# Kernel optimization log

Hardware: AMD Instinct MI355X
Metric: run time of the kernel (lower is better)

## Reference

```python
import jax, jax.numpy as jnp
import numpy as np

B, N, FH, H, FO = 8, 1024, 128, 8, 64
FIN = 2 * FH  # f_hid * 2
NEG = -1e9
SLOPE = 0.2  # leaky_relu negative slope (GAT default)


def setup_inputs() -> dict:
    key = jax.random.key(0)
    ks = jax.random.split(key, 10)
    x = jax.random.normal(ks[0], (B, FIN), jnp.float32)
    A = jax.random.randint(ks[1], (B, N, N), 0, 2, jnp.int32)  # 0/1 dense adjacency
    mask_zero = jnp.ones((B, N, 1), jnp.float32)  # node validity mask
    p_atten = jax.random.uniform(ks[2], (B, N), jnp.float32)  # unused in forward body
    e_atten = jax.random.uniform(ks[3], (B, N, FIN), jnp.float32)
    Npost = jax.random.normal(ks[4], (N, FIN), jnp.float32) * np.float32(1.0 / np.sqrt(FIN))  # kaiming-ish
    w = jax.random.normal(ks[5], (H, FIN, FO), jnp.float32) * np.float32(1.0 / np.sqrt(FIN))
    a_src = jax.random.normal(ks[6], (H, FO), jnp.float32) * np.float32(0.1)
    a_dst = jax.random.normal(ks[7], (H, FO), jnp.float32) * np.float32(0.1)
    bias = jnp.zeros((FO,), jnp.float32)
    return {"x": x, "A": A, "mask_zero": mask_zero, "p_atten": p_atten,
            "e_atten": e_atten, "Npost": Npost, "w": w, "a_src": a_src,
            "a_dst": a_dst, "bias": bias}


def reference(x, A, mask_zero, p_atten, e_atten, Npost, w, a_src, a_dst, bias):
    # broadcast-mul feature gating: x [B,FIN] repeated over N posts, gated by Npost*e_atten
    recx = x[:, None, :] * (Npost[None, :, :] * e_atten)          # [B,N,FIN]
    # BatchGAT (DeepInf-style multi-head graph attention, dropout disabled / eval mode)
    h = jnp.einsum('bnf,hfo->bhno', recx, w)                      # [B,H,N,FO]
    s = jnp.einsum('bhno,ho->bhn', h, a_src)                      # src attention term
    d = jnp.einsum('bhno,ho->bhn', h, a_dst)                      # dst attention term
    logits = jax.nn.leaky_relu(s[:, :, :, None] + d[:, :, None, :], SLOPE)  # [B,H,N,N]
    adj = (A > 0)[:, None, :, :]                                  # [B,1,N,N]
    logits = jnp.where(adj, logits, NEG)
    attn = jax.nn.softmax(logits, axis=-1)                        # masked row softmax
    out = jnp.einsum('bhnm,bhmo->bhno', attn, h) + bias           # aggregate neighbors
    out = out.mean(axis=1)                                        # average heads -> [B,N,FO]
    return out * mask_zero                                        # zero padded nodes
```

## Files before the change

kernel.cpp:

```cpp
#include <hip/hip_runtime.h>

typedef __attribute__((ext_vector_type(8))) short          bf16x8;
typedef __attribute__((ext_vector_type(8))) unsigned short u16x8;
typedef __attribute__((ext_vector_type(4))) unsigned short u16x4;
typedef __attribute__((ext_vector_type(4))) float          f32x4;
typedef __attribute__((ext_vector_type(4))) unsigned int   u32x4;

union U8 { u16x8 u; bf16x8 b; u32x4 w; };
union U4 { u16x4 u; unsigned w[2]; };

__device__ __forceinline__ unsigned short f2bf(float f){
  unsigned u = __float_as_uint(f);
  return (unsigned short)((u + 0x7fffu + ((u >> 16) & 1u)) >> 16);
}
__device__ __forceinline__ unsigned pack_bf16(float lo, float hi){
  unsigned a = __float_as_uint(hi) + 0x8000u;
  unsigned b = __float_as_uint(lo) + 0x8000u;
  return __builtin_amdgcn_perm(a, b, 0x07060302u);
}

#define NN  1024
#define FIN 256
#define NH  8
#define FO  64

__global__ __launch_bounds__(256) void stage0(
    const float* __restrict__ w, const int* __restrict__ A,
    const float* __restrict__ bias, const float* __restrict__ mz,
    unsigned short* __restrict__ wfrag, unsigned long long* __restrict__ Abits,
    float* __restrict__ out)
{
  const int tid = blockIdx.x * 256 + threadIdx.x;
  if (tid < 16384){
    const int lane = tid & 63, ss = (tid >> 6) & 3, kc = (tid >> 8) & 7, h = tid >> 11;
    const int o = 16 * ss + (lane & 15);
    const int f = kc * 32 + (lane >> 4) * 8;
    u16x8 r;
    #pragma unroll
    for (int j = 0; j < 8; j++) r[j] = f2bf(w[(h * FIN + f + j) * FO + o]);
    *(u16x8*)(wfrag + tid * 8) = r;
  }
  #pragma unroll
  for (int k = 0; k < 2; k++){
    const int i = tid + k * 262144;
    out[i] = bias[i & 63] * mz[i >> 6];
  }
  for (int i = tid; i < 8388608; i += 262144){
    unsigned long long m = __ballot(A[i] > 0);
    if ((threadIdx.x & 63) == 0) Abits[i >> 6] = m;
  }
}

__global__ __launch_bounds__(512, 4) void stageA(
    const float* __restrict__ x, const float* __restrict__ e_at,
    const float* __restrict__ Np, const unsigned short* __restrict__ wfrag,
    const float* __restrict__ a_src, const float* __restrict__ a_dst,
    unsigned short* __restrict__ hT,
    float* __restrict__ exps, float* __restrict__ exps2,
    float* __restrict__ expd, float* __restrict__ expd2)
{
  __shared__ unsigned short rex[16 * 264];
  const int t = threadIdx.x;
  const int n0 = blockIdx.x * 16, b = blockIdx.y;

  {
    const int row = t >> 5, f0 = (t & 31) * 8;
    const int nrow = n0 + row;
    const float* ep = e_at + (b * NN + nrow) * FIN + f0;
    const float* qp = Np + nrow * FIN + f0;
    const float* xp = x + b * FIN + f0;
    f32x4 e0 = *(const f32x4*)ep, e1 = *(const f32x4*)(ep + 4);
    f32x4 q0 = *(const f32x4*)qp, q1 = *(const f32x4*)(qp + 4);
    f32x4 x0 = *(const f32x4*)xp, x1 = *(const f32x4*)(xp + 4);
    u16x8 r;
    #pragma unroll
    for (int j = 0; j < 4; j++){
      r[j]     = f2bf(e0[j] * q0[j] * x0[j]);
      r[j + 4] = f2bf(e1[j] * q1[j] * x1[j]);
    }
    *(u16x8*)(rex + row * 264 + f0) = r;
  }
  __syncthreads();

  const int h = t >> 6, lane = t & 63, quad = lane >> 4, l15 = lane & 15;
  const unsigned short* wf = wfrag + h * 16384 + lane * 8;

  f32x4 acc[4] = {};
  #pragma unroll
  for (int kc = 0; kc < 8; kc++){
    U8 a0, bf[4];
    a0.u = *(const u16x8*)(rex + l15 * 264 + kc * 32 + quad * 8);
    #pragma unroll
    for (int ss = 0; ss < 4; ss++) bf[ss].u = *(const u16x8*)(wf + (kc * 4 + ss) * 512);
    #pragma unroll
    for (int ss = 0; ss < 4; ss++)
      acc[ss] = __builtin_amdgcn_mfma_f32_16x16x32_bf16(a0.b, bf[ss].b, acc[ss], 0, 0, 0);
  }

  {
    const int mtile = blockIdx.x >> 1, moff = (blockIdx.x & 1) * 16;
    unsigned short* pan = hT + (size_t)(((b * NH + h) * 32 + mtile) * 64) * 32;
    #pragma unroll
    for (int ss = 0; ss < 4; ss++){
      U4 v;
      v.w[0] = pack_bf16(acc[ss][0], acc[ss][1]);
      v.w[1] = pack_bf16(acc[ss][2], acc[ss][3]);
      *(u16x4*)(pan + (16 * ss + l15) * 32 + moff + quad * 4) = v.u;
    }
  }

  float as4[4], ad4[4];
  #pragma unroll
  for (int ss = 0; ss < 4; ss++){
    as4[ss] = a_src[h * FO + 16 * ss + l15];
    ad4[ss] = a_dst[h * FO + 16 * ss + l15];
  }
  #pragma unroll
  for (int i = 0; i < 4; i++){
    float ps = 0.f, pd = 0.f;
    #pragma unroll
    for (int ss = 0; ss < 4; ss++){ ps += acc[ss][i] * as4[ss]; pd += acc[ss][i] * ad4[ss]; }
    #pragma unroll
    for (int off = 1; off < 16; off <<= 1){
      ps += __shfl_xor(ps, off);
      pd += __shfl_xor(pd, off);
    }
    if (l15 == 0){
      const int idx = (b * NH + h) * NN + n0 + quad * 4 + i;
      exps [idx] = __expf(ps);
      exps2[idx] = __expf(0.2f * ps);
      expd [idx] = __expf(pd);
      expd2[idx] = __expf(0.2f * pd);
    }
  }
}

__global__ __launch_bounds__(512, 8) void stageB(
    const unsigned* __restrict__ Aw,
    const unsigned short* __restrict__ hT,
    const float* __restrict__ exps, const float* __restrict__ exps2,
    const float* __restrict__ expd, const float* __restrict__ expd2,
    const float* __restrict__ mz, float* __restrict__ out)
{
  __shared__ float ed_l[2 * NN];
  __shared__ float e2_l[2 * NN];
  __shared__ unsigned mask_l[32 * 33];
  __shared__ float l_l[4 * 16];
  const int t = threadIdx.x;
  const int n0 = blockIdx.x * 32, hq = blockIdx.y, b = blockIdx.z;
  const int w = t >> 6, lane = t & 63, quad = lane >> 4, l15 = lane & 15;
  const int hl = w & 1, rg = (w >> 1) & 1, mh = w >> 2;
  const int h = hq * 2 + hl;

  if (t < 64) l_l[t] = 0.f;
  {
    const float* s1 = expd  + (b * NH + hq * 2) * NN;
    const float* s2 = expd2 + (b * NH + hq * 2) * NN;
    *(f32x4*)(ed_l + t * 4) = *(const f32x4*)(s1 + t * 4);
    *(f32x4*)(e2_l + t * 4) = *(const f32x4*)(s2 + t * 4);
  }
  #pragma unroll
  for (int k = 0; k < 2; k++){
    const int i = t + k * 512;
    mask_l[(i >> 5) * 33 + (i & 31)] = Aw[(b * NN + n0 + (i >> 5)) * 32 + (i & 31)];
  }
  __syncthreads();

  const int hb = (b * NH + h) * NN;
  const float Es  = exps [hb + n0 + rg * 16 + l15];
  const float Es2 = exps2[hb + n0 + rg * 16 + l15];
  const unsigned short* pb = hT + (size_t)(b * NH + h) * 65536 + l15 * 32 + quad * 8;
  const float* edh = ed_l + hl * NN + quad * 8;
  const float* e2h = e2_l + hl * NN + quad * 8;
  const unsigned* maskp = mask_l + (rg * 16 + l15) * 33;
  const int c0 = mh * 16;

  U8 pan[4];
  #pragma unroll
  for (int ss = 0; ss < 4; ss++)
    pan[ss].u = *(const u16x8*)(pb + (size_t)c0 * 2048 + ss * 512);

  f32x4 acc[4] = {};
  float lp = 0.f;

  for (int cc = 0; cc < 16; cc++){
    const int c = c0 + cc;
    const unsigned am = maskp[c] >> (quad * 8);
    float pv[8];
    #pragma unroll
    for (int g2 = 0; g2 < 2; g2++){
      f32x4 dv = *(const f32x4*)(edh + c * 32 + g2 * 4);
      f32x4 gv = *(const f32x4*)(e2h + c * 32 + g2 * 4);
      #pragma unroll
      for (int j = 0; j < 4; j++){
        float e = fmaxf(Es * dv[j], Es2 * gv[j]);
        pv[g2 * 4 + j] = (am & (1u << (g2 * 4 + j))) ? e : 0.f;
      }
    }
    lp += ((pv[0] + pv[1]) + (pv[2] + pv[3])) + ((pv[4] + pv[5]) + (pv[6] + pv[7]));
    U8 p;
    #pragma unroll
    for (int r = 0; r < 4; r++) p.w[r] = pack_bf16(pv[2 * r], pv[2 * r + 1]);
    #pragma unroll
    for (int ss = 0; ss < 4; ss++)
      acc[ss] = __builtin_amdgcn_mfma_f32_16x16x32_bf16(p.b, pan[ss].b, acc[ss], 0, 0, 0);
    if (cc + 1 < 16){
      #pragma unroll
      for (int ss = 0; ss < 4; ss++)
        pan[ss].u = *(const u16x8*)(pb + (size_t)(c + 1) * 2048 + ss * 512);
    }
  }

  lp += __shfl_xor(lp, 16);
  lp += __shfl_xor(lp, 32);
  if (lane < 16) atomicAdd(&l_l[(w & 3) * 16 + lane], lp);
  __syncthreads();

  const float* mzp = mz + b * NN + n0 + rg * 16;
  #pragma unroll
  for (int i = 0; i < 4; i++){
    const int row = quad * 4 + i;
    const float invm = (0.125f / l_l[(w & 3) * 16 + row]) * mzp[row];
    float* op = out + (size_t)(b * NN + n0 + rg * 16 + row) * FO + l15;
    #pragma unroll
    for (int ss = 0; ss < 4; ss++)
      atomicAdd(op + ss * 16, acc[ss][i] * invm);
  }
}

extern "C" void kernel_launch(void* const* d_in, const int* in_sizes, int n_in,
                              void* d_out, int out_size, void* d_ws, size_t ws_size,
                              hipStream_t stream)
{
  (void)in_sizes; (void)n_in; (void)out_size; (void)ws_size;
  const float* x    = (const float*)d_in[0];
  const int*   A    = (const int*)d_in[1];
  const float* mz   = (const float*)d_in[2];
  const float* e_at = (const float*)d_in[4];
  const float* Np   = (const float*)d_in[5];
  const float* w    = (const float*)d_in[6];
  const float* asrc = (const float*)d_in[7];
  const float* adst = (const float*)d_in[8];
  const float* bias = (const float*)d_in[9];
  float* out = (float*)d_out;

  char* ws = (char*)d_ws;
  unsigned short* wfrag = (unsigned short*)ws;
  unsigned short* hT    = (unsigned short*)(ws + 262144);
  float* exps  = (float*)(ws + 8650752);
  float* exps2 = (float*)(ws + 8912896);
  float* expd  = (float*)(ws + 9175040);
  float* expd2 = (float*)(ws + 9437184);
  unsigned long long* Abits = (unsigned long long*)(ws + 9699328);

  stage0<<<dim3(1024), dim3(256), 0, stream>>>(w, A, bias, mz, wfrag, Abits, out);
  stageA<<<dim3(64, 8), dim3(512), 0, stream>>>(x, e_at, Np, wfrag, asrc, adst,
                                                hT, exps, exps2, expd, expd2);
  stageB<<<dim3(32, 4, 8), dim3(512), 0, stream>>>((const unsigned*)Abits, hT,
                                                   exps, exps2, expd, expd2,
                                                   mz, out);
}
```

Measured before the change: 168.6 us.

## Precompute 16-bit adjacency masks, fold exp ratio, compute row sums via MFMA

```diff
diff --git a/kernel.cpp b/kernel.cpp
--- a/kernel.cpp
+++ b/kernel.cpp
@@ -18,6 +18,11 @@
   unsigned b = __float_as_uint(lo) + 0x8000u;
   return __builtin_amdgcn_perm(a, b, 0x07060302u);
 }
+__device__ __forceinline__ unsigned maskpack(float e0, float e1, unsigned m){
+  unsigned r;
+  asm("v_cvt_pk_bf16_f32 %0, %1, %2" : "=v"(r) : "v"(e0), "v"(e1));
+  return r & m;
+}
 
 #define NN  1024
 #define FIN 256
@@ -27,7 +32,7 @@
 __global__ __launch_bounds__(256) void stage0(
     const float* __restrict__ w, const int* __restrict__ A,
     const float* __restrict__ bias, const float* __restrict__ mz,
-    unsigned short* __restrict__ wfrag, unsigned long long* __restrict__ Abits,
+    unsigned short* __restrict__ wfrag, unsigned* __restrict__ emask,
     float* __restrict__ out)
 {
   const int tid = blockIdx.x * 256 + threadIdx.x;
@@ -45,9 +50,15 @@
     const int i = tid + k * 262144;
     out[i] = bias[i & 63] * mz[i >> 6];
   }
-  for (int i = tid; i < 8388608; i += 262144){
-    unsigned long long m = __ballot(A[i] > 0);
-    if ((threadIdx.x & 63) == 0) Abits[i >> 6] = m;
+  const int4* A4 = (const int4*)A;
+  for (int i = tid; i < 1048576; i += 262144){
+    const int4 a0 = A4[2 * i], a1 = A4[2 * i + 1];
+    u32x4 m;
+    m[0] = (a0.x > 0 ? 0xFFFFu : 0u) | (a0.y > 0 ? 0xFFFF0000u : 0u);
+    m[1] = (a0.z > 0 ? 0xFFFFu : 0u) | (a0.w > 0 ? 0xFFFF0000u : 0u);
+    m[2] = (a1.x > 0 ? 0xFFFFu : 0u) | (a1.y > 0 ? 0xFFFF0000u : 0u);
+    m[3] = (a1.z > 0 ? 0xFFFFu : 0u) | (a1.w > 0 ? 0xFFFF0000u : 0u);
+    *(u32x4*)(emask + 4 * i) = m;
   }
 }
 
@@ -56,8 +67,7 @@
     const float* __restrict__ Np, const unsigned short* __restrict__ wfrag,
     const float* __restrict__ a_src, const float* __restrict__ a_dst,
     unsigned short* __restrict__ hT,
-    float* __restrict__ exps, float* __restrict__ exps2,
-    float* __restrict__ expd, float* __restrict__ expd2)
+    float* __restrict__ Rt, float* __restrict__ expd, float* __restrict__ expd2)
 {
   __shared__ unsigned short rex[16 * 264];
   const int t = threadIdx.x;
@@ -127,24 +137,22 @@
     }
     if (l15 == 0){
       const int idx = (b * NH + h) * NN + n0 + quad * 4 + i;
-      exps [idx] = __expf(ps);
-      exps2[idx] = __expf(0.2f * ps);
-      expd [idx] = __expf(pd);
+      Rt[idx]    = __expf(0.8f * ps);
+      expd[idx]  = __expf(pd);
       expd2[idx] = __expf(0.2f * pd);
     }
   }
 }
 
 __global__ __launch_bounds__(512, 8) void stageB(
-    const unsigned* __restrict__ Aw,
+    const unsigned* __restrict__ emask,
     const unsigned short* __restrict__ hT,
-    const float* __restrict__ exps, const float* __restrict__ exps2,
+    const float* __restrict__ Rt,
     const float* __restrict__ expd, const float* __restrict__ expd2,
     const float* __restrict__ mz, float* __restrict__ out)
 {
   __shared__ float ed_l[2 * NN];
   __shared__ float e2_l[2 * NN];
-  __shared__ unsigned mask_l[32 * 33];
   __shared__ float l_l[4 * 16];
   const int t = threadIdx.x;
   const int n0 = blockIdx.x * 32, hq = blockIdx.y, b = blockIdx.z;
@@ -159,69 +167,66 @@
     *(f32x4*)(ed_l + t * 4) = *(const f32x4*)(s1 + t * 4);
     *(f32x4*)(e2_l + t * 4) = *(const f32x4*)(s2 + t * 4);
   }
-  #pragma unroll
-  for (int k = 0; k < 2; k++){
-    const int i = t + k * 512;
-    mask_l[(i >> 5) * 33 + (i & 31)] = Aw[(b * NN + n0 + (i >> 5)) * 32 + (i & 31)];
-  }
   __syncthreads();
 
-  const int hb = (b * NH + h) * NN;
-  const float Es  = exps [hb + n0 + rg * 16 + l15];
-  const float Es2 = exps2[hb + n0 + rg * 16 + l15];
+  const int row = n0 + rg * 16 + l15;
+  const float Rv = Rt[(b * NH + h) * NN + row];
   const unsigned short* pb = hT + (size_t)(b * NH + h) * 65536 + l15 * 32 + quad * 8;
   const float* edh = ed_l + hl * NN + quad * 8;
   const float* e2h = e2_l + hl * NN + quad * 8;
-  const unsigned* maskp = mask_l + (rg * 16 + l15) * 33;
+  const unsigned* emp = emask + ((size_t)(b * NN) + row) * 512 + quad * 4;
   const int c0 = mh * 16;
 
   U8 pan[4];
   #pragma unroll
   for (int ss = 0; ss < 4; ss++)
     pan[ss].u = *(const u16x8*)(pb + (size_t)c0 * 2048 + ss * 512);
+  u32x4 em = *(const u32x4*)(emp + c0 * 16);
+
+  U8 ones;
+  #pragma unroll
+  for (int j = 0; j < 8; j++) ones.u[j] = 0x3F80;
 
   f32x4 acc[4] = {};
-  float lp = 0.f;
+  f32x4 accl = {};
 
   for (int cc = 0; cc < 16; cc++){
     const int c = c0 + cc;
-    const unsigned am = maskp[c] >> (quad * 8);
-    float pv[8];
-    #pragma unroll
-    for (int g2 = 0; g2 < 2; g2++){
-      f32x4 dv = *(const f32x4*)(edh + c * 32 + g2 * 4);
-      f32x4 gv = *(const f32x4*)(e2h + c * 32 + g2 * 4);
-      #pragma unroll
-      for (int j = 0; j < 4; j++){
-        float e = fmaxf(Es * dv[j], Es2 * gv[j]);
-        pv[g2 * 4 + j] = (am & (1u << (g2 * 4 + j))) ? e : 0.f;
-      }
-    }
-    lp += ((pv[0] + pv[1]) + (pv[2] + pv[3])) + ((pv[4] + pv[5]) + (pv[6] + pv[7]));
+    f32x4 d01 = *(const f32x4*)(edh + c * 32);
+    f32x4 d23 = *(const f32x4*)(edh + c * 32 + 4);
+    f32x4 g01 = *(const f32x4*)(e2h + c * 32);
+    f32x4 g23 = *(const f32x4*)(e2h + c * 32 + 4);
+    f32x4 p01 = Rv * d01, p23 = Rv * d23;
     U8 p;
-    #pragma unroll
-    for (int r = 0; r < 4; r++) p.w[r] = pack_bf16(pv[2 * r], pv[2 * r + 1]);
+    p.w[0] = maskpack(fmaxf(p01[0], g01[0]), fmaxf(p01[1], g01[1]), em[0]);
+    p.w[1] = maskpack(fmaxf(p01[2], g01[2]), fmaxf(p01[3], g01[3]), em[1]);
+    p.w[2] = maskpack(fmaxf(p23[0], g23[0]), fmaxf(p23[1], g23[1]), em[2]);
+    p.w[3] = maskpack(fmaxf(p23[2], g23[2]), fmaxf(p23[3], g23[3]), em[3]);
     #pragma unroll
     for (int ss = 0; ss < 4; ss++)
       acc[ss] = __builtin_amdgcn_mfma_f32_16x16x32_bf16(p.b, pan[ss].b, acc[ss], 0, 0, 0);
+    accl = __builtin_amdgcn_mfma_f32_16x16x32_bf16(p.b, ones.b, accl, 0, 0, 0);
     if (cc + 1 < 16){
       #pragma unroll
       for (int ss = 0; ss < 4; ss++)
         pan[ss].u = *(const u16x8*)(pb + (size_t)(c + 1) * 2048 + ss * 512);
-    }
-  }
-
-  lp += __shfl_xor(lp, 16);
-  lp += __shfl_xor(lp, 32);
-  if (lane < 16) atomicAdd(&l_l[(w & 3) * 16 + lane], lp);
+      em = *(const u32x4*)(emp + (c + 1) * 16);
+    }
+  }
+
+  if (l15 == 0){
+    #pragma unroll
+    for (int i = 0; i < 4; i++)
+      atomicAdd(&l_l[(w & 3) * 16 + quad * 4 + i], accl[i]);
+  }
   __syncthreads();
 
   const float* mzp = mz + b * NN + n0 + rg * 16;
   #pragma unroll
   for (int i = 0; i < 4; i++){
-    const int row = quad * 4 + i;
-    const float invm = (0.125f / l_l[(w & 3) * 16 + row]) * mzp[row];
-    float* op = out + (size_t)(b * NN + n0 + rg * 16 + row) * FO + l15;
+    const int r = quad * 4 + i;
+    const float invm = (0.125f / l_l[(w & 3) * 16 + r]) * mzp[r];
+    float* op = out + (size_t)(b * NN + n0 + rg * 16 + r) * FO + l15;
     #pragma unroll
     for (int ss = 0; ss < 4; ss++)
       atomicAdd(op + ss * 16, acc[ss][i] * invm);
@@ -247,16 +252,14 @@
   char* ws = (char*)d_ws;
   unsigned short* wfrag = (unsigned short*)ws;
   unsigned short* hT    = (unsigned short*)(ws + 262144);
-  float* exps  = (float*)(ws + 8650752);
-  float* exps2 = (float*)(ws + 8912896);
-  float* expd  = (float*)(ws + 9175040);
-  float* expd2 = (float*)(ws + 9437184);
-  unsigned long long* Abits = (unsigned long long*)(ws + 9699328);
-
-  stage0<<<dim3(1024), dim3(256), 0, stream>>>(w, A, bias, mz, wfrag, Abits, out);
+  float* Rt    = (float*)(ws + 8650752);
+  float* expd  = (float*)(ws + 8912896);
+  float* expd2 = (float*)(ws + 9175040);
+  unsigned* emask = (unsigned*)(ws + 9437184);
+
+  stage0<<<dim3(1024), dim3(256), 0, stream>>>(w, A, bias, mz, wfrag, emask, out);
   stageA<<<dim3(64, 8), dim3(512), 0, stream>>>(x, e_at, Np, wfrag, asrc, adst,
-                                                hT, exps, exps2, expd, expd2);
-  stageB<<<dim3(32, 4, 8), dim3(512), 0, stream>>>((const unsigned*)Abits, hT,
-                                                   exps, exps2, expd, expd2,
+                                                hT, Rt, expd, expd2);
+  stageB<<<dim3(32, 4, 8), dim3(512), 0, stream>>>(emask, hT, Rt, expd, expd2,
                                                    mz, out);
 }
```

Result: slower. 178.7 us (+6.0%).
